# Performance work log

Measured on AMD Instinct MI355X. Metric: run time of the kernel, lower is better.

## Reference

```python
import jax, jax.numpy as jnp
import numpy as np


def setup_inputs() -> dict:
    key = jax.random.key(0)
    ks = jax.random.split(key, 8)
    B, C, H, W = 4, 128, 64, 64
    C8 = C // 8
    return {
        "x": jax.random.normal(ks[0], (B, C, H, W), dtype=jnp.float32),
        "Wq": jax.random.normal(ks[1], (C8, C), dtype=jnp.float32) * (1.0 / np.sqrt(C)),
        "bq": jax.random.normal(ks[2], (C8,), dtype=jnp.float32) * 0.01,
        "Wk": jax.random.normal(ks[3], (C8, C), dtype=jnp.float32) * (1.0 / np.sqrt(C)),
        "bk": jax.random.normal(ks[4], (C8,), dtype=jnp.float32) * 0.01,
        "Wv": jax.random.normal(ks[5], (C, C), dtype=jnp.float32) * (1.0 / np.sqrt(C)),
        "bv": jax.random.normal(ks[6], (C,), dtype=jnp.float32) * 0.01,
        "gamma": jax.random.normal(ks[7], (1,), dtype=jnp.float32),
    }


def reference(x, Wq, bq, Wk, bk, Wv, bv, gamma):
    B, C, H, W = x.shape
    N = H * W
    xf = x.reshape(B, C, N)  # flatten spatial dims; 1x1 conv == channel matmul
    q = jnp.einsum("oc,bcn->bon", Wq, xf) + bq[None, :, None]  # (B, C8, N)
    k = jnp.einsum("oc,bcn->bon", Wk, xf) + bk[None, :, None]  # (B, C8, N)
    v = jnp.einsum("oc,bcn->bon", Wv, xf) + bv[None, :, None]  # (B, C, N)
    scores = jnp.einsum("bci,bcj->bij", q, k)  # (B, N, N), query rows x key cols
    attn = jax.nn.softmax(scores, axis=-1)
    out = jnp.einsum("bcj,bij->bci", v, attn)  # (B, C, N)
    out = out.reshape(B, C, H, W)
    return gamma[0] * out + x
```

## Files before the change

kernel.cpp:

```cpp
#include <hip/hip_runtime.h>
#include <math.h>

typedef __attribute__((ext_vector_type(8))) short bf16x8;
typedef __attribute__((ext_vector_type(16))) float f32x16;

constexpr int Bn = 4, Cn = 128, C8n = 16, Nn = 4096;

#if __has_builtin(__builtin_amdgcn_exp2f)
#define EXP2F(x) __builtin_amdgcn_exp2f(x)
#else
#define EXP2F(x) exp2f(x)
#endif

__device__ inline unsigned short f2bf(float f) {
    unsigned u = __builtin_bit_cast(unsigned, f);
    u += 0x7fff + ((u >> 16) & 1);
    return (unsigned short)(u >> 16);
}
__device__ inline unsigned pack2(float a, float b) {
    return (unsigned)f2bf(a) | ((unsigned)f2bf(b) << 16);
}
__device__ inline unsigned pkt(float a, float b) {
#if __has_builtin(__builtin_amdgcn_perm)
    return __builtin_amdgcn_perm(__builtin_bit_cast(unsigned, b),
                                 __builtin_bit_cast(unsigned, a), 0x07060302u);
#else
    return (__builtin_bit_cast(unsigned, a) >> 16) |
           (__builtin_bit_cast(unsigned, b) & 0xffff0000u);
#endif
}

__global__ __launch_bounds__(256) void qkv_kernel(
    const float* __restrict__ x,
    const float* __restrict__ Wq, const float* __restrict__ bq,
    const float* __restrict__ Wk, const float* __restrict__ bk,
    const float* __restrict__ Wv, const float* __restrict__ bv,
    unsigned short* __restrict__ qT, unsigned short* __restrict__ kT,
    unsigned short* __restrict__ vsw)
{
    __shared__ unsigned short wlds[160 * 128];
    __shared__ unsigned short v_s[128 * 64];
    __shared__ float qk_s[32][65];
    __shared__ float bfl[160];

    const int tid = threadIdx.x;
    const int b = blockIdx.x >> 6, n0 = (blockIdx.x & 63) << 6;
    const int w = tid >> 6, lane = tid & 63, col = lane & 31, half = lane >> 5;
    const float L2E = 1.4426950408889634f;

    {
        unsigned* wl32 = (unsigned*)wlds;
        for (int i = tid; i < 160 * 32; i += 256) {
            int r = i >> 5, cq = (i & 31) << 2;
            const float* src; float sc = 1.0f;
            if (r < 16)      { src = Wq + (size_t)r * Cn;        sc = L2E; }
            else if (r < 32) { src = Wk + (size_t)(r - 16) * Cn; }
            else             { src = Wv + (size_t)(r - 32) * Cn; }
            float4 t = *reinterpret_cast<const float4*>(&src[cq]);
            int G = cq >> 3;
            unsigned* wp = wl32 + 64 * r + 4 * (G ^ (r & 7)) + ((cq & 7) >> 1);
            wp[0] = pack2(t.x * sc, t.y * sc);
            wp[1] = pack2(t.z * sc, t.w * sc);
        }
        if (tid < 160)
            bfl[tid] = (tid < 16) ? bq[tid] * L2E
                     : (tid < 32) ? bk[tid - 16] : bv[tid - 32];
    }

    const int nx = n0 + ((w & 1) << 5);
    const float* xb = x + ((size_t)b * Cn) * Nn + nx + col;
    bf16x8 af[8];
    #pragma unroll
    for (int s = 0; s < 8; ++s) {
        float v[8];
        #pragma unroll
        for (int j = 0; j < 8; ++j)
            v[j] = xb[(size_t)(16 * s + 8 * half + j) * Nn];
        uint4 u = make_uint4(pack2(v[0], v[1]), pack2(v[2], v[3]),
                             pack2(v[4], v[5]), pack2(v[6], v[7]));
        af[s] = __builtin_bit_cast(bf16x8, u);
    }
    __syncthreads();

    const int mb = (w >> 1) ? 3 : 0;
    const bool three = (w >> 1) == 0;
    f32x16 a0, a1, a2;
    {
        float b0 = bfl[32 * mb + col], b1 = bfl[32 * (mb + 1) + col];
        float b2v = three ? bfl[64 + col] : 0.0f;
        #pragma unroll
        for (int r = 0; r < 16; ++r) { a0[r] = b0; a1[r] = b1; a2[r] = b2v; }
    }
    #pragma unroll
    for (int s = 0; s < 8; ++s) {
        const int off = 8 * ((2 * s + half) ^ (col & 7));
        a0 = __builtin_amdgcn_mfma_f32_32x32x16_bf16(af[s],
             *(const bf16x8*)(wlds + 128 * (32 * mb + col) + off), a0, 0, 0, 0);
        a1 = __builtin_amdgcn_mfma_f32_32x32x16_bf16(af[s],
             *(const bf16x8*)(wlds + 128 * (32 * (mb + 1) + col) + off), a1, 0, 0, 0);
        if (three)
            a2 = __builtin_amdgcn_mfma_f32_32x32x16_bf16(af[s],
                 *(const bf16x8*)(wlds + 128 * (64 + col) + off), a2, 0, 0, 0);
    }

    unsigned* vp32 = (unsigned*)v_s;
    #define VS_WRITE(A, C0) { \
        const int c_ = (C0) + col; \
        _Pragma("unroll") for (int g = 0; g < 4; ++g) { \
            int Gn = ((w & 1) << 2) + g; \
            unsigned* up = vp32 + 32 * c_ + 4 * (Gn ^ (c_ & 7)) + (half << 1); \
            up[0] = pack2(A[4 * g],     A[4 * g + 1]); \
            up[1] = pack2(A[4 * g + 2], A[4 * g + 3]); } }

    if (w < 2) {
        #pragma unroll
        for (int r = 0; r < 16; ++r)
            qk_s[col][((w & 1) << 5) + (r & 3) + ((r >> 2) << 3) + (half << 2)] = a0[r];
        VS_WRITE(a1, 0)
        VS_WRITE(a2, 32)
    } else {
        VS_WRITE(a0, 64)
        VS_WRITE(a1, 96)
    }
    #undef VS_WRITE
    __syncthreads();

    if (tid < 128) {
        int n = tid & 63, which = tid >> 6;
        unsigned wv_[8];
        #pragma unroll
        for (int i = 0; i < 8; ++i)
            wv_[i] = pack2(qk_s[16 * which + 2 * i][n], qk_s[16 * which + 2 * i + 1][n]);
        unsigned short* dst = (which ? kT : qT) + ((size_t)b * Nn + n0 + n) * C8n;
        *reinterpret_cast<uint4*>(dst)     = make_uint4(wv_[0], wv_[1], wv_[2], wv_[3]);
        *reinterpret_cast<uint4*>(dst + 8) = make_uint4(wv_[4], wv_[5], wv_[6], wv_[7]);
    }
    {
        const int ct = w, c_ = (ct << 5) + col;
        #pragma unroll
        for (int t = 0; t < 4; ++t) {
            int Gn = (t << 1) + half;
            bf16x8 fr = *(const bf16x8*)(vp32 + 32 * c_ + 4 * (Gn ^ (c_ & 7)));
            size_t o_ = ((((size_t)b * 256 + (n0 >> 4) + t) * 4 + ct) * 64 + lane) * 8;
            *reinterpret_cast<uint4*>(&vsw[o_]) = __builtin_bit_cast(uint4, fr);
        }
    }
}

__global__ __launch_bounds__(512) void attn_kernel(
    const unsigned short* __restrict__ qT, const unsigned short* __restrict__ kT,
    const unsigned short* __restrict__ vsw, const float* __restrict__ x,
    const float* __restrict__ gamma_p, float* __restrict__ out)
{
    __shared__ unsigned sm_u32[8192];
    __shared__ float ls[2][2][64];
    __shared__ float invl[64];

    const int tid = threadIdx.x, wv = tid >> 6, lane = tid & 63;
    const int col = lane & 31, half = lane >> 5;
    const int xcd = blockIdx.x & 7;
    const int b = xcd >> 1;
    const int q0 = ((((blockIdx.x >> 3) << 1) | (xcd & 1))) << 6;

    const unsigned short* qb = qT + (size_t)b * Nn * C8n;
    bf16x8 qf0 = *(const bf16x8*)&qb[(size_t)(q0 + col) * C8n + 8 * half];
    bf16x8 qf1 = *(const bf16x8*)&qb[(size_t)(q0 + 32 + col) * C8n + 8 * half];

    f32x16 accA[4], accB[4];
    #pragma unroll
    for (int ct = 0; ct < 4; ++ct) { accA[ct] = {}; accB[ct] = {}; }
    float l0 = 0.0f, l1 = 0.0f;
    const unsigned short* kb = kT + (size_t)b * Nn * C8n;

#if __has_builtin(__builtin_amdgcn_permlane32_swap)
    #define MKPF(P, O, F) { \
        unsigned lo0 = pkt(P[O], P[O + 1]), lo1 = pkt(P[O + 2], P[O + 3]); \
        unsigned hi0 = pkt(P[O + 4], P[O + 5]), hi1 = pkt(P[O + 6], P[O + 7]); \
        auto r0 = __builtin_amdgcn_permlane32_swap(lo0, hi0, false, false); \
        auto r1 = __builtin_amdgcn_permlane32_swap(lo1, hi1, false, false); \
        uint4 u_ = make_uint4(r0[0], r1[0], r0[1], r1[1]); \
        F = __builtin_bit_cast(bf16x8, u_); }
#else
    #define MKPF(P, O, F) { \
        unsigned lo0 = pkt(P[O], P[O + 1]), lo1 = pkt(P[O + 2], P[O + 3]); \
        unsigned hi0 = pkt(P[O + 4], P[O + 5]), hi1 = pkt(P[O + 6], P[O + 7]); \
        unsigned t0 = half ? lo0 : hi0, t1 = half ? lo1 : hi1; \
        unsigned r0 = (unsigned)__shfl_xor((int)t0, 32); \
        unsigned r1 = (unsigned)__shfl_xor((int)t1, 32); \
        uint4 u_ = make_uint4(half ? r0 : lo0, half ? r1 : lo1, \
                              half ? hi0 : r0, half ? hi1 : r1); \
        F = __builtin_bit_cast(bf16x8, u_); }
#endif

    #pragma unroll 1
    for (int kt = 0; kt < 16; ++kt) {
        const int j0 = (wv << 9) + (kt << 5);
        const size_t vbase = ((((size_t)b * 256 + (j0 >> 4)) * 4) * 64 + lane) * 8;
        bf16x8 va[4], vb2[4];
        #pragma unroll
        for (int ct = 0; ct < 4; ++ct) {
            va[ct]  = *(const bf16x8*)&vsw[vbase + (size_t)ct * 512];
            vb2[ct] = *(const bf16x8*)&vsw[vbase + (size_t)(4 + ct) * 512];
        }
        bf16x8 kf = *(const bf16x8*)&kb[(size_t)(j0 + col) * C8n + 8 * half];
        f32x16 z = {};

        {
            f32x16 s = __builtin_amdgcn_mfma_f32_32x32x16_bf16(kf, qf0, z, 0, 0, 0);
            float p[16]; float ps = 0.0f;
            #pragma unroll
            for (int r = 0; r < 16; ++r) { p[r] = EXP2F(s[r]); ps += p[r]; }
            l0 += ps;
            bf16x8 pf0, pf1;
            MKPF(p, 0, pf0) MKPF(p, 8, pf1)
            __builtin_amdgcn_s_setprio(1);
            #pragma unroll
            for (int ct = 0; ct < 4; ++ct) {
                accA[ct] = __builtin_amdgcn_mfma_f32_32x32x16_bf16(va[ct],  pf0, accA[ct], 0, 0, 0);
                accA[ct] = __builtin_amdgcn_mfma_f32_32x32x16_bf16(vb2[ct], pf1, accA[ct], 0, 0, 0);
            }
            __builtin_amdgcn_s_setprio(0);
        }
        {
            f32x16 s = __builtin_amdgcn_mfma_f32_32x32x16_bf16(kf, qf1, z, 0, 0, 0);
            float p[16]; float ps = 0.0f;
            #pragma unroll
            for (int r = 0; r < 16; ++r) { p[r] = EXP2F(s[r]); ps += p[r]; }
            l1 += ps;
            bf16x8 pf0, pf1;
            MKPF(p, 0, pf0) MKPF(p, 8, pf1)
            __builtin_amdgcn_s_setprio(1);
            #pragma unroll
            for (int ct = 0; ct < 4; ++ct) {
                accB[ct] = __builtin_amdgcn_mfma_f32_32x32x16_bf16(va[ct],  pf0, accB[ct], 0, 0, 0);
                accB[ct] = __builtin_amdgcn_mfma_f32_32x32x16_bf16(vb2[ct], pf1, accB[ct], 0, 0, 0);
            }
            __builtin_amdgcn_s_setprio(0);
        }
    }
    #undef MKPF

    l0 += __shfl_xor(l0, 32);
    l1 += __shfl_xor(l1, 32);

    #define SL_STORE(SL) { \
        ls[SL][0][lane] = l0; ls[SL][1][lane] = l1; \
        unsigned* sb = sm_u32 + (SL) * 4096; \
        _Pragma("unroll") for (int ct = 0; ct < 4; ++ct) \
        _Pragma("unroll") for (int i = 0; i < 8; ++i) { \
            sb[((ct) * 8 + i) * 64 + lane]     = pkt(accA[ct][2 * i], accA[ct][2 * i + 1]); \
            sb[((4 + ct) * 8 + i) * 64 + lane] = pkt(accB[ct][2 * i], accB[ct][2 * i + 1]); } }
    #define SL_ADD(SL) { \
        l0 += ls[SL][0][lane]; l1 += ls[SL][1][lane]; \
        unsigned* sb = sm_u32 + (SL) * 4096; \
        _Pragma("unroll") for (int ct = 0; ct < 4; ++ct) \
        _Pragma("unroll") for (int i = 0; i < 8; ++i) { \
            unsigned ua = sb[((ct) * 8 + i) * 64 + lane]; \
            accA[ct][2 * i]     += __builtin_bit_cast(float, ua << 16); \
            accA[ct][2 * i + 1] += __builtin_bit_cast(float, ua & 0xffff0000u); \
            unsigned ub = sb[((4 + ct) * 8 + i) * 64 + lane]; \
            accB[ct][2 * i]     += __builtin_bit_cast(float, ub << 16); \
            accB[ct][2 * i + 1] += __builtin_bit_cast(float, ub & 0xffff0000u); } }
    #define SL_RMW(SL) { \
        ls[SL][0][lane] += l0; ls[SL][1][lane] += l1; \
        unsigned* sb = sm_u32 + (SL) * 4096; \
        _Pragma("unroll") for (int ct = 0; ct < 4; ++ct) \
        _Pragma("unroll") for (int i = 0; i < 8; ++i) { \
            unsigned ua = sb[((ct) * 8 + i) * 64 + lane]; \
            float x0 = __builtin_bit_cast(float, ua << 16) + accA[ct][2 * i]; \
            float x1 = __builtin_bit_cast(float, ua & 0xffff0000u) + accA[ct][2 * i + 1]; \
            sb[((ct) * 8 + i) * 64 + lane] = pkt(x0, x1); \
            unsigned ub = sb[((4 + ct) * 8 + i) * 64 + lane]; \
            float y0 = __builtin_bit_cast(float, ub << 16) + accB[ct][2 * i]; \
            float y1 = __builtin_bit_cast(float, ub & 0xffff0000u) + accB[ct][2 * i + 1]; \
            sb[((4 + ct) * 8 + i) * 64 + lane] = pkt(y0, y1); } }

    if (wv == 4 || wv == 5) SL_STORE(wv - 4)
    __syncthreads();
    if (wv == 0 || wv == 1) SL_ADD(wv)
    __syncthreads();
    if (wv == 6 || wv == 7) SL_STORE(wv - 6)
    __syncthreads();
    if (wv == 2 || wv == 3) SL_RMW(wv - 2)
    __syncthreads();
    if (wv == 0 || wv == 1) SL_ADD(wv)
    __syncthreads();
    if (wv == 1) SL_STORE(0)
    __syncthreads();
    float* sf = (float*)sm_u32;
    if (wv == 0) {
        SL_ADD(0)
        #pragma unroll
        for (int ct = 0; ct < 4; ++ct)
            #pragma unroll
            for (int r = 0; r < 16; ++r) {
                sf[((ct) * 16 + r) * 64 + lane]     = accA[ct][r];
                sf[((4 + ct) * 16 + r) * 64 + lane] = accB[ct][r];
            }
        if (lane < 32) { invl[col] = 1.0f / l0; invl[32 + col] = 1.0f / l1; }
    }
    __syncthreads();
    #undef SL_STORE
    #undef SL_ADD
    #undef SL_RMW

    {
        const float g = gamma_p[0];
        const int n = tid & 63, ci = tid >> 6;
        const float il = invl[n];
        const int qs = n >> 5, nc = n & 31;
        #pragma unroll
        for (int p = 0; p < 16; ++p) {
            int ch = (p << 3) + ci;
            int ct = ch >> 5, chl = ch & 31;
            int h = (chl >> 2) & 1, r = (chl & 3) | ((chl >> 3) << 2);
            float val = sf[((qs * 4 + ct) * 16 + r) * 64 + nc + (h << 5)];
            size_t idx = ((size_t)(b * Cn + ch)) * Nn + q0 + n;
            out[idx] = g * (val * il) + x[idx];
        }
    }
}

extern "C" void kernel_launch(void* const* d_in, const int* in_sizes, int n_in,
                              void* d_out, int out_size, void* d_ws, size_t ws_size,
                              hipStream_t stream)
{
    const float* x     = (const float*)d_in[0];
    const float* Wq    = (const float*)d_in[1];
    const float* bq    = (const float*)d_in[2];
    const float* Wk    = (const float*)d_in[3];
    const float* bk    = (const float*)d_in[4];
    const float* Wv    = (const float*)d_in[5];
    const float* bv    = (const float*)d_in[6];
    const float* gamma = (const float*)d_in[7];
    float* out = (float*)d_out;

    unsigned short* ws16 = (unsigned short*)d_ws;
    unsigned short* qTw  = ws16;
    unsigned short* kTw  = qTw + (size_t)Bn * Nn * C8n;
    unsigned short* vsww = kTw + (size_t)Bn * Nn * C8n;

    qkv_kernel<<<dim3(256), dim3(256), 0, stream>>>(
        x, Wq, bq, Wk, bk, Wv, bv, qTw, kTw, vsww);

    attn_kernel<<<dim3(256), dim3(512), 0, stream>>>(
        qTw, kTw, vsww, x, gamma, out);
}
```

Baseline: 111.8 us.

## Split QKV projection across two grid rows and prefetch next K fragment

The QKV projection kernel now launches twice as many blocks: one row computes Q, K and the first half of V, the other computes the second half of V. This halves the per-block weight staging, LDS use and MFMA work, so more blocks can run at once. The cost is that each x tile is loaded and converted twice. The x loads are also issued before weight staging so they overlap, and the attention loop now loads the next key fragment one iteration ahead to hide its latency.

```diff
diff --git a/kernel.cpp b/kernel.cpp
--- a/kernel.cpp
+++ b/kernel.cpp
@@ -38,69 +38,74 @@
     unsigned short* __restrict__ qT, unsigned short* __restrict__ kT,
     unsigned short* __restrict__ vsw)
 {
-    __shared__ unsigned short wlds[160 * 128];
-    __shared__ unsigned short v_s[128 * 64];
+    __shared__ unsigned short wlds[96 * 128];
+    __shared__ unsigned short v_s[64 * 64];
     __shared__ float qk_s[32][65];
-    __shared__ float bfl[160];
+    __shared__ float bfl[96];
 
     const int tid = threadIdx.x;
     const int b = blockIdx.x >> 6, n0 = (blockIdx.x & 63) << 6;
+    const int y = blockIdx.y;
     const int w = tid >> 6, lane = tid & 63, col = lane & 31, half = lane >> 5;
+    const int g01 = w >> 1;
     const float L2E = 1.4426950408889634f;
+    const int RBASE = y ? 96 : 0;
+    const int RCNT  = y ? 64 : 96;
+
+    const int nx = n0 + ((w & 1) << 5);
+    const float* xb = x + ((size_t)b * Cn) * Nn + nx + col;
+    bf16x8 af[8];
+    #pragma unroll
+    for (int s = 0; s < 8; ++s) {
+        float v[8];
+        #pragma unroll
+        for (int j = 0; j < 8; ++j)
+            v[j] = xb[(size_t)(16 * s + 8 * half + j) * Nn];
+        uint4 u = make_uint4(pack2(v[0], v[1]), pack2(v[2], v[3]),
+                             pack2(v[4], v[5]), pack2(v[6], v[7]));
+        af[s] = __builtin_bit_cast(bf16x8, u);
+    }
 
     {
         unsigned* wl32 = (unsigned*)wlds;
-        for (int i = tid; i < 160 * 32; i += 256) {
-            int r = i >> 5, cq = (i & 31) << 2;
+        for (int i = tid; i < RCNT * 32; i += 256) {
+            int rl = i >> 5, cq = (i & 31) << 2;
+            int r = RBASE + rl;
             const float* src; float sc = 1.0f;
             if (r < 16)      { src = Wq + (size_t)r * Cn;        sc = L2E; }
             else if (r < 32) { src = Wk + (size_t)(r - 16) * Cn; }
             else             { src = Wv + (size_t)(r - 32) * Cn; }
             float4 t = *reinterpret_cast<const float4*>(&src[cq]);
             int G = cq >> 3;
-            unsigned* wp = wl32 + 64 * r + 4 * (G ^ (r & 7)) + ((cq & 7) >> 1);
+            unsigned* wp = wl32 + 64 * rl + 4 * (G ^ (rl & 7)) + ((cq & 7) >> 1);
             wp[0] = pack2(t.x * sc, t.y * sc);
             wp[1] = pack2(t.z * sc, t.w * sc);
         }
-        if (tid < 160)
-            bfl[tid] = (tid < 16) ? bq[tid] * L2E
-                     : (tid < 32) ? bk[tid - 16] : bv[tid - 32];
-    }
-
-    const int nx = n0 + ((w & 1) << 5);
-    const float* xb = x + ((size_t)b * Cn) * Nn + nx + col;
-    bf16x8 af[8];
-    #pragma unroll
-    for (int s = 0; s < 8; ++s) {
-        float v[8];
-        #pragma unroll
-        for (int j = 0; j < 8; ++j)
-            v[j] = xb[(size_t)(16 * s + 8 * half + j) * Nn];
-        uint4 u = make_uint4(pack2(v[0], v[1]), pack2(v[2], v[3]),
-                             pack2(v[4], v[5]), pack2(v[6], v[7]));
-        af[s] = __builtin_bit_cast(bf16x8, u);
-    }
-    __syncthreads();
-
-    const int mb = (w >> 1) ? 3 : 0;
-    const bool three = (w >> 1) == 0;
-    f32x16 a0, a1, a2;
+        if (tid < RCNT) {
+            int r = RBASE + tid;
+            bfl[tid] = (r < 16) ? bq[r] * L2E
+                     : (r < 32) ? bk[r - 16] : bv[r - 32];
+        }
+    }
+    __syncthreads();
+
+    const int mlA = (y == 0) ? (g01 ? 2 : 0) : g01;
+    const bool hasB = (y == 0) && (g01 == 0);
+    f32x16 a0, a1;
     {
-        float b0 = bfl[32 * mb + col], b1 = bfl[32 * (mb + 1) + col];
-        float b2v = three ? bfl[64 + col] : 0.0f;
-        #pragma unroll
-        for (int r = 0; r < 16; ++r) { a0[r] = b0; a1[r] = b1; a2[r] = b2v; }
+        float b0 = bfl[32 * mlA + col];
+        float b1 = hasB ? bfl[32 + col] : 0.0f;
+        #pragma unroll
+        for (int r = 0; r < 16; ++r) { a0[r] = b0; a1[r] = b1; }
     }
     #pragma unroll
     for (int s = 0; s < 8; ++s) {
         const int off = 8 * ((2 * s + half) ^ (col & 7));
         a0 = __builtin_amdgcn_mfma_f32_32x32x16_bf16(af[s],
-             *(const bf16x8*)(wlds + 128 * (32 * mb + col) + off), a0, 0, 0, 0);
-        a1 = __builtin_amdgcn_mfma_f32_32x32x16_bf16(af[s],
-             *(const bf16x8*)(wlds + 128 * (32 * (mb + 1) + col) + off), a1, 0, 0, 0);
-        if (three)
-            a2 = __builtin_amdgcn_mfma_f32_32x32x16_bf16(af[s],
-                 *(const bf16x8*)(wlds + 128 * (64 + col) + off), a2, 0, 0, 0);
+             *(const bf16x8*)(wlds + 128 * (32 * mlA + col) + off), a0, 0, 0, 0);
+        if (hasB)
+            a1 = __builtin_amdgcn_mfma_f32_32x32x16_bf16(af[s],
+                 *(const bf16x8*)(wlds + 128 * (32 + col) + off), a1, 0, 0, 0);
     }
 
     unsigned* vp32 = (unsigned*)v_s;
@@ -112,20 +117,23 @@
             up[0] = pack2(A[4 * g],     A[4 * g + 1]); \
             up[1] = pack2(A[4 * g + 2], A[4 * g + 3]); } }
 
-    if (w < 2) {
-        #pragma unroll
-        for (int r = 0; r < 16; ++r)
-            qk_s[col][((w & 1) << 5) + (r & 3) + ((r >> 2) << 3) + (half << 2)] = a0[r];
-        VS_WRITE(a1, 0)
-        VS_WRITE(a2, 32)
+    if (y == 0) {
+        if (g01 == 0) {
+            #pragma unroll
+            for (int r = 0; r < 16; ++r)
+                qk_s[col][((w & 1) << 5) + (r & 3) + ((r >> 2) << 3) + (half << 2)] = a0[r];
+            VS_WRITE(a1, 0)
+        } else {
+            VS_WRITE(a0, 32)
+        }
     } else {
-        VS_WRITE(a0, 64)
-        VS_WRITE(a1, 96)
+        if (g01 == 0) { VS_WRITE(a0, 0)  }
+        else          { VS_WRITE(a0, 32) }
     }
     #undef VS_WRITE
     __syncthreads();
 
-    if (tid < 128) {
+    if (y == 0 && tid < 128) {
         int n = tid & 63, which = tid >> 6;
         unsigned wv_[8];
         #pragma unroll
@@ -136,12 +144,14 @@
         *reinterpret_cast<uint4*>(dst + 8) = make_uint4(wv_[4], wv_[5], wv_[6], wv_[7]);
     }
     {
-        const int ct = w, c_ = (ct << 5) + col;
-        #pragma unroll
-        for (int t = 0; t < 4; ++t) {
+        const int ctl = w & 1, c_ = (ctl << 5) + col;
+        const int tb = (w >> 1) << 1;
+        #pragma unroll
+        for (int tt = 0; tt < 2; ++tt) {
+            int t = tb + tt;
             int Gn = (t << 1) + half;
             bf16x8 fr = *(const bf16x8*)(vp32 + 32 * c_ + 4 * (Gn ^ (c_ & 7)));
-            size_t o_ = ((((size_t)b * 256 + (n0 >> 4) + t) * 4 + ct) * 64 + lane) * 8;
+            size_t o_ = ((((size_t)b * 256 + (n0 >> 4) + t) * 4 + ((y << 1) | ctl)) * 64 + lane) * 8;
             *reinterpret_cast<uint4*>(&vsw[o_]) = __builtin_bit_cast(uint4, fr);
         }
     }
@@ -192,9 +202,13 @@
         F = __builtin_bit_cast(bf16x8, u_); }
 #endif
 
+    bf16x8 kf = *(const bf16x8*)&kb[(size_t)((wv << 9) + col) * C8n + 8 * half];
+
     #pragma unroll 1
     for (int kt = 0; kt < 16; ++kt) {
         const int j0 = (wv << 9) + (kt << 5);
+        const int j0n = (wv << 9) + (((kt + 1) & 15) << 5);
+        bf16x8 kf_next = *(const bf16x8*)&kb[(size_t)(j0n + col) * C8n + 8 * half];
         const size_t vbase = ((((size_t)b * 256 + (j0 >> 4)) * 4) * 64 + lane) * 8;
         bf16x8 va[4], vb2[4];
         #pragma unroll
@@ -202,7 +216,6 @@
             va[ct]  = *(const bf16x8*)&vsw[vbase + (size_t)ct * 512];
             vb2[ct] = *(const bf16x8*)&vsw[vbase + (size_t)(4 + ct) * 512];
         }
-        bf16x8 kf = *(const bf16x8*)&kb[(size_t)(j0 + col) * C8n + 8 * half];
         f32x16 z = {};
 
         {
@@ -237,6 +250,7 @@
             }
             __builtin_amdgcn_s_setprio(0);
         }
+        kf = kf_next;
     }
     #undef MKPF
 
@@ -340,7 +354,7 @@
     unsigned short* kTw  = qTw + (size_t)Bn * Nn * C8n;
     unsigned short* vsww = kTw + (size_t)Bn * Nn * C8n;
 
-    qkv_kernel<<<dim3(256), dim3(256), 0, stream>>>(
+    qkv_kernel<<<dim3(256, 2), dim3(256), 0, stream>>>(
         x, Wq, bq, Wk, bk, Wv, bv, qTw, kTw, vsww);
 
     attn_kernel<<<dim3(256), dim3(512), 0, stream>>>(
```

Result: faster. 107.7 us (-3.7%).
